# Kernel tuning notes

Measured on AMD Instinct MI355X. Metric: run time of the kernel, lower is better.

## Reference

```python
import jax, jax.numpy as jnp
import numpy as np

B, N, D, H, A = 1024, 8, 256, 512, 4  # batch, num_objects, embedding_dim, hidden_dim, action_dim


def _edge_list(batch, n):
    # Fully connected (no self-loops) over n nodes, replicated per sample with offset b*n.
    pairs = np.array([(i, j) for i in range(n) for j in range(n) if i != j], dtype=np.int32)
    off = (np.arange(batch, dtype=np.int32) * n)[:, None]
    row = (pairs[:, 0][None, :] + off).reshape(-1)
    col = (pairs[:, 1][None, :] + off).reshape(-1)
    return jnp.asarray(row), jnp.asarray(col)


def _layer_norm(x, g, b):
    m = x.mean(-1, keepdims=True)
    v = x.var(-1, keepdims=True)
    return (x - m) / jnp.sqrt(v + 1e-5) * g + b


def _mlp(x, w1, b1, w2, b2, g, bn, w3, b3):
    h = jax.nn.relu(x @ w1 + b1)
    h = jax.nn.relu(_layer_norm(h @ w2 + b2, g, bn))
    return h @ w3 + b3


def setup_inputs() -> dict:
    key = jax.random.key(0)
    ks = jax.random.split(key, 12)
    def w(k, shape):
        return jax.random.normal(k, shape, jnp.float32) / np.sqrt(shape[0]).astype(np.float32)
    return {
        "states": jax.random.normal(ks[0], (B, N, D), jnp.float32),
        "action": jax.random.randint(ks[1], (B,), 0, A),
        # edge MLP: 3D -> H -> H (LN) -> H
        "e_w1": w(ks[2], (3 * D, H)), "e_b1": jnp.zeros((H,), jnp.float32),
        "e_w2": w(ks[3], (H, H)),     "e_b2": jnp.zeros((H,), jnp.float32),
        "e_g":  jnp.ones((H,), jnp.float32), "e_bn": jnp.zeros((H,), jnp.float32),
        "e_w3": w(ks[4], (H, H)),     "e_b3": jnp.zeros((H,), jnp.float32),
        # node MLP: H + D + A -> H -> H (LN) -> D
        "n_w1": w(ks[5], (H + D + A, H)), "n_b1": jnp.zeros((H,), jnp.float32),
        "n_w2": w(ks[6], (H, H)),         "n_b2": jnp.zeros((H,), jnp.float32),
        "n_g":  jnp.ones((H,), jnp.float32), "n_bn": jnp.zeros((H,), jnp.float32),
        "n_w3": w(ks[7], (H, D)),         "n_b3": jnp.zeros((D,), jnp.float32),
    }


def reference(states, action,
              e_w1, e_b1, e_w2, e_b2, e_g, e_bn, e_w3, e_b3,
              n_w1, n_b1, n_w2, n_b2, n_g, n_bn, n_w3, n_b3):
    eP = (e_w1, e_b1, e_w2, e_b2, e_g, e_bn, e_w3, e_b3)
    nP = (n_w1, n_b1, n_w2, n_b2, n_g, n_bn, n_w3, n_b3)
    flat = states.reshape(-1, D)                       # [B*N, D]
    row, col = _edge_list(B, N - 1)                    # faithful: edge list over N-1 objects
    E = row.shape[0]
    # copy_action / embodied: one-hot action repeated per object
    av = jnp.repeat(jax.nn.one_hot(action, A, dtype=flat.dtype), N, axis=0)  # [B*N, A]
    # round 0: edge_attr starts as zeros like node features
    e = _mlp(jnp.concatenate([flat[row], jnp.zeros((E, D), flat.dtype), flat[col]], 1), *eP)
    agg = jax.ops.segment_sum(e, row, num_segments=B * N)  # [B*N, H]
    node = _mlp(jnp.concatenate([flat, av, agg], 1), *nP)   # [B*N, D]
    flat = flat + node
    av0 = jnp.zeros_like(av)
    for _ in range(N - 1):
        e = _mlp(jnp.concatenate([flat[row], node[row], flat[col]], 1), *eP)
        agg = jax.ops.segment_sum(e, row, num_segments=B * N)
        node = _mlp(jnp.concatenate([flat, av0, agg], 1), *nP)
        flat = flat + node
    return flat.reshape(B, N, D)
```

## Files before the change

kernel.cpp:

```cpp
#include <hip/hip_runtime.h>
#include <cstddef>

typedef _Float16 f16x8 __attribute__((ext_vector_type(8)));
typedef _Float16 f16x4 __attribute__((ext_vector_type(4)));
typedef float f32x16 __attribute__((ext_vector_type(16)));
typedef unsigned short ushort_t;

#define NSEG 7168
#define NNODE 8192

enum { EP_NONE = 0, EP_BIAS = 1, EP_RAWP = 2, EP_NL1 = 3, EP_NL3 = 4 };

#define PHASE_BARRIER() do { asm volatile("s_waitcnt lgkmcnt(0)" ::: "memory"); \
                             __builtin_amdgcn_s_barrier(); } while (0)

#define RELU8(v) do { _Pragma("unroll") \
  for (int j_ = 0; j_ < 8; ++j_) v[j_] = v[j_] > (_Float16)0 ? v[j_] : (_Float16)0; } while (0)

__global__ __launch_bounds__(256)
void prepack(const float* __restrict__ W, ushort_t* __restrict__ P,
             int koff, int kcnt, int Nsrc, int NTpack, int noff) {
  int idx = blockIdx.x * 256 + threadIdx.x;
  if (idx >= kcnt * Nsrc) return;
  int kl = idx / Nsrc, n = idx - kl * Nsrc + noff;
  _Float16 h = (_Float16)W[idx];
  int k = koff + kl;
  size_t o = ((((size_t)(k >> 4)) * NTpack + (n >> 5)) * 64 + ((k >> 3) & 1) * 32 + (n & 31)) * 8 + (k & 7);
  P[o] = __builtin_bit_cast(ushort_t, h);
}

__global__ __launch_bounds__(256)
void v6k(const float* __restrict__ eb3, const float* __restrict__ nw1,
         float* __restrict__ v6) {
  int n = blockIdx.x * 256 + threadIdx.x;
  if (n >= 512) return;
  float a = 0.f;
  for (int k = 0; k < 512; ++k) a += eb3[k] * nw1[(size_t)(260 + k) * 512 + n];
  v6[n] = 6.f * a;
}

template <int NCOLB, int EPI, int EDGE, int LNIN, int X1F16, int OUTF16>
__global__ __launch_bounds__(256, 4)
void gemmT(const void* __restrict__ X1v, int ld1, int nph1,
           const void* __restrict__ X2v, int ld2, int nph2,
           const ushort_t* __restrict__ Sm, const ushort_t* __restrict__ Tm,
           const ushort_t* __restrict__ P,
           const float* __restrict__ bias, const float* __restrict__ bias2,
           const int* __restrict__ action, const float* __restrict__ wact,
           const float* __restrict__ lnpart,
           const float* __restrict__ lng, const float* __restrict__ lnbn,
           void* __restrict__ Yv, float* __restrict__ Yres,
           float* __restrict__ Part, int m0base) {
  constexpr int N = NCOLB * 128;
  constexpr int NT = N / 32;
  const int u = threadIdx.x;
  const int nwg = gridDim.x;
  const int qq = nwg >> 3, r8 = nwg & 7;
  const int xcd = blockIdx.x & 7, inx = blockIdx.x >> 3;
  const int logical = (xcd < r8 ? xcd * (qq + 1) : r8 * (qq + 1) + (xcd - r8) * qq) + inx;
  const int mY = (logical / NCOLB) * 64;
  const int cb = logical - (logical / NCOLB) * NCOLB;
  const int nB = cb * 128;
  const int lane = u & 63, w = u >> 6;
  const int wr = w >> 1, wc = w & 1;
  const int r31 = lane & 31, rt2 = lane >> 5;

  __shared__ ushort_t lA[16384];
  __shared__ int eR[64], eC[64];

  if (EDGE) {
    if (u < 64) {
      int e = m0base + mY + u;
      int b = e / 42, p = e - b * 42;
      int i = p / 6, tt = p - i * 6;
      int j = tt + (tt >= i ? 1 : 0);
      eR[u] = b * 7 + i;
      eC[u] = b * 7 + j;
    }
    __syncthreads();
  }

  const int kcA = w * 2, kcB = w * 2 + 1;
  const int widx0 = (((rt2 * 8 + kcA) * 2 + 0) * 32 + (r31 ^ ((kcA & 3) << 3))) * 8;
  const int widx1 = (((rt2 * 8 + kcA) * 2 + 1) * 32 + (r31 ^ ((kcA & 3) << 3))) * 8;
  const int widx2 = (((rt2 * 8 + kcB) * 2 + 0) * 32 + (r31 ^ ((kcB & 3) << 3))) * 8;
  const int widx3 = (((rt2 * 8 + kcB) * 2 + 1) * 32 + (r31 ^ ((kcB & 3) << 3))) * 8;

  const ushort_t* sB = nullptr;
  const ushort_t* tB = nullptr;
  const float* x1f = nullptr;
  const ushort_t* x1h = nullptr;
  const ushort_t* x2h = nullptr;
  if (EDGE) {
    sB = Sm + (size_t)eR[lane] * 1024 + w * 32;
    tB = Tm + (size_t)eC[lane] * 1024 + w * 32;
  } else {
    if (X1F16) x1h = (const ushort_t*)X1v + (size_t)(mY + lane) * ld1 + w * 32;
    else       x1f = (const float*)X1v + (size_t)(mY + lane) * ld1 + w * 32;
    if (nph2 > 0) x2h = (const ushort_t*)X2v + (size_t)(mY + lane) * ld2 + w * 32;
  }
  float mym = 0.f, myr = 0.f;
  if (LNIN) {
    const float* pp = lnpart + (size_t)(mY + lane) * 16;
    float S_ = 0.f, Q_ = 0.f;
    #pragma unroll
    for (int i = 0; i < 8; ++i) { S_ += pp[i]; Q_ += pp[8 + i]; }
    mym = S_ * (1.f / 512.f);
    myr = rsqrtf(Q_ * (1.f / 512.f) - mym * mym + 1e-5f);
  }

  f16x8 xc0, xc1, xc2, xc3;
  auto loadx = [&](int ph) {
    if (EDGE) {
      const ushort_t* sp = sB + ph * 128;
      const ushort_t* tp = tB + ph * 128;
      f16x8 s0 = *(const f16x8*)sp,        t0 = *(const f16x8*)tp;
      f16x8 s1 = *(const f16x8*)(sp + 8),  t1 = *(const f16x8*)(tp + 8);
      f16x8 s2 = *(const f16x8*)(sp + 16), t2 = *(const f16x8*)(tp + 16);
      f16x8 s3 = *(const f16x8*)(sp + 24), t3 = *(const f16x8*)(tp + 24);
      xc0 = s0 + t0; xc1 = s1 + t1; xc2 = s2 + t2; xc3 = s3 + t3;
      RELU8(xc0); RELU8(xc1); RELU8(xc2); RELU8(xc3);
    } else if (!X1F16 && ph < nph1) {
      const float* src = x1f + ph * 128;
      float4 l0 = *(const float4*)(src +  0), h0 = *(const float4*)(src +  4);
      float4 l1 = *(const float4*)(src +  8), h1 = *(const float4*)(src + 12);
      float4 l2 = *(const float4*)(src + 16), h2 = *(const float4*)(src + 20);
      float4 l3 = *(const float4*)(src + 24), h3 = *(const float4*)(src + 28);
#define CVT8(X, lo, hi) do { X[0]=(_Float16)lo.x; X[1]=(_Float16)lo.y; \
      X[2]=(_Float16)lo.z; X[3]=(_Float16)lo.w; X[4]=(_Float16)hi.x; \
      X[5]=(_Float16)hi.y; X[6]=(_Float16)hi.z; X[7]=(_Float16)hi.w; } while (0)
      CVT8(xc0, l0, h0); CVT8(xc1, l1, h1); CVT8(xc2, l2, h2); CVT8(xc3, l3, h3);
#undef CVT8
    } else {
      const ushort_t* src = (ph < nph1) ? x1h + ph * 128 : x2h + (ph - nph1) * 128;
      xc0 = *(const f16x8*)src;
      xc1 = *(const f16x8*)(src + 8);
      xc2 = *(const f16x8*)(src + 16);
      xc3 = *(const f16x8*)(src + 24);
      if (LNIN) {
        const int kb = ph * 128 + w * 32;
#define LN8(X, OFS) do { _Pragma("unroll") for (int j_ = 0; j_ < 8; ++j_) { \
        float xx = (float)X[j_]; \
        xx = fmaxf((xx - mym) * myr * lng[kb + (OFS) + j_] + lnbn[kb + (OFS) + j_], 0.f); \
        X[j_] = (_Float16)xx; } } while (0)
        LN8(xc0, 0); LN8(xc1, 8); LN8(xc2, 16); LN8(xc3, 24);
#undef LN8
      }
    }
  };
  auto cvtwrite = [&](int b) {
    const int base = b * 8192;
    *(f16x8*)&lA[base + widx0] = xc0;
    *(f16x8*)&lA[base + widx1] = xc1;
    *(f16x8*)&lA[base + widx2] = xc2;
    *(f16x8*)&lA[base + widx3] = xc3;
  };

  f32x16 acc0, acc1;
  #pragma unroll
  for (int q = 0; q < 16; ++q) { acc0[q] = 0.f; acc1[q] = 0.f; }

  const int nph = nph1 + nph2;
  const int ntb = (nB >> 5) + wc * 2;
  const int TOT = nph * 8;

#define LOADA(S, A_) do { \
    const int aofs_ = lbase + (((wr * 8 + (S)) * 2 + rt2) * 32 + (r31 ^ (((S) & 3) << 3))) * 8; \
    A_ = *(const f16x8*)&lA[aofs_]; } while (0)

#define LOADB(G_, H0, H1) do { \
    const ushort_t* bp_ = P + (((size_t)(G_) * NT + ntb) * 64 + lane) * 8; \
    H0 = *(const f16x8*)bp_; \
    H1 = *(const f16x8*)(bp_ + 512); } while (0)

#define MFMA2(AH, H0, H1) do { \
    acc0 = __builtin_amdgcn_mfma_f32_32x32x16_f16(AH, H0, acc0, 0, 0, 0); \
    acc1 = __builtin_amdgcn_mfma_f32_32x32x16_f16(AH, H1, acc1, 0, 0, 0); } while (0)

  loadx(0);
  cvtwrite(0);
  if (nph > 1) loadx(1);
  PHASE_BARRIER();
  f16x8 b00, b01, b10, b11, b20, b21, b30, b31;
  LOADB(0, b00, b01);
  LOADB(1, b10, b11);
  LOADB(2, b20, b21);
  LOADB(3, b30, b31);

  #pragma unroll 1
  for (int ph = 0; ph < nph; ++ph) {
    if (ph + 1 < nph) {
      cvtwrite((ph + 1) & 1);
      if (ph + 2 < nph) loadx(ph + 2);
    }
    const int lbase = (ph & 1) * 8192;
    const int g0 = ph * 8;
    f16x8 ac, an;
    LOADA(0, ac);
#define STEP(S, BH, BL) do { \
    if ((S) < 7) LOADA((S) + 1, an); \
    f16x8 h0 = BH, h1 = BL; \
    if (g0 + (S) + 4 < TOT) LOADB(g0 + (S) + 4, BH, BL); \
    MFMA2(ac, h0, h1); \
    if ((S) < 7) ac = an; } while (0)
    STEP(0, b00, b01);
    STEP(1, b10, b11);
    STEP(2, b20, b21);
    STEP(3, b30, b31);
    STEP(4, b00, b01);
    STEP(5, b10, b11);
    STEP(6, b20, b21);
    STEP(7, b30, b31);
#undef STEP
    if (ph + 1 < nph) PHASE_BARRIER();
  }

  const int col0 = nB + wc * 64 + r31;
  float v[2][16];
  {
    float bc0 = (EPI == EP_NONE) ? 0.f : bias[col0];
    float bc1 = (EPI == EP_NONE) ? 0.f : bias[col0 + 32];
    #pragma unroll
    for (int q = 0; q < 16; ++q) {
      v[0][q] = acc0[q] + bc0;
      v[1][q] = acc1[q] + bc1;
    }
  }

  if (EPI == EP_NL1) {
    #pragma unroll
    for (int q = 0; q < 16; ++q) {
      int m = mY + wr * 32 + (q & 3) + 8 * (q >> 2) + 4 * rt2;
      if (m < NSEG) {
        v[0][q] += bias2[col0];
        v[1][q] += bias2[col0 + 32];
      }
      if (action != nullptr) {
        const float* wrp = wact + (size_t)(256 + action[m >> 3]) * 512;
        v[0][q] += wrp[col0];
        v[1][q] += wrp[col0 + 32];
      }
    }
    #pragma unroll
    for (int ct = 0; ct < 2; ++ct)
      #pragma unroll
      for (int q = 0; q < 16; ++q) v[ct][q] = fmaxf(v[ct][q], 0.f);
  }

  if (EPI == EP_RAWP) {
    float sv[16], qv[16];
    #pragma unroll
    for (int q = 0; q < 16; ++q) {
      sv[q] = v[0][q] + v[1][q];
      qv[q] = v[0][q] * v[0][q] + v[1][q] * v[1][q];
    }
    #pragma unroll
    for (int mm = 1; mm <= 16; mm <<= 1) {
      #pragma unroll
      for (int q = 0; q < 16; ++q) {
        sv[q] += __shfl_xor(sv[q], mm);
        qv[q] += __shfl_xor(qv[q], mm);
      }
    }
    if (r31 == 0) {
      #pragma unroll
      for (int q = 0; q < 16; ++q) {
        int m = mY + wr * 32 + (q & 3) + 8 * (q >> 2) + 4 * rt2;
        Part[(size_t)m * 16 + cb * 2 + wc] = sv[q];
        Part[(size_t)m * 16 + 8 + cb * 2 + wc] = qv[q];
      }
    }
  }

  #pragma unroll
  for (int ct = 0; ct < 2; ++ct) {
    #pragma unroll
    for (int q = 0; q < 16; ++q) {
      int m = mY + wr * 32 + (q & 3) + 8 * (q >> 2) + 4 * rt2;
      float z = v[ct][q];
      if (OUTF16)
        ((ushort_t*)Yv)[(size_t)m * N + col0 + ct * 32] =
            __builtin_bit_cast(ushort_t, (_Float16)z);
      else
        ((float*)Yv)[(size_t)m * N + col0 + ct * 32] = z;
      if (EPI == EP_NL3) Yres[(size_t)m * N + col0 + ct * 32] += z;
    }
  }
#undef LOADA
#undef LOADB
#undef MFMA2
}

__global__ __launch_bounds__(256)
void h2_sum_ln(const ushort_t* __restrict__ H2, const float* __restrict__ Part,
               const float* __restrict__ g, const float* __restrict__ bn,
               ushort_t* __restrict__ SS) {
  __shared__ float smu[12], srs[12];
  const int u = threadIdx.x;
  const int g2 = blockIdx.x * 2;
  if (u < 12) {
    const float* pp = Part + ((size_t)g2 * 6 + u) * 16;
    float S = 0.f, Q = 0.f;
    #pragma unroll
    for (int i = 0; i < 8; ++i) { S += pp[i]; Q += pp[8 + i]; }
    float m = S * (1.f / 512.f);
    smu[u] = m;
    srs[u] = rsqrtf(Q * (1.f / 512.f) - m * m + 1e-5f);
  }
  __syncthreads();
  const int ln = g2 + (u >> 7);
  const int lloc = (u >> 7) * 6;
  const int c4 = (u & 127) * 4;
  float4 gv = *(const float4*)(g + c4);
  float4 bv = *(const float4*)(bn + c4);
  float a0 = 0.f, a1 = 0.f, a2 = 0.f, a3 = 0.f;
  #pragma unroll
  for (int r = 0; r < 6; ++r) {
    int row = ln * 6 + r;
    f16x4 y = *(const f16x4*)(H2 + (size_t)row * 512 + c4);
    float m = smu[lloc + r], rs = srs[lloc + r];
    a0 += fmaxf(((float)y[0] - m) * rs * gv.x + bv.x, 0.f);
    a1 += fmaxf(((float)y[1] - m) * rs * gv.y + bv.y, 0.f);
    a2 += fmaxf(((float)y[2] - m) * rs * gv.z + bv.z, 0.f);
    a3 += fmaxf(((float)y[3] - m) * rs * gv.w + bv.w, 0.f);
  }
  f16x4 o;
  o[0] = (_Float16)a0; o[1] = (_Float16)a1; o[2] = (_Float16)a2; o[3] = (_Float16)a3;
  *(f16x4*)(SS + (size_t)ln * 512 + c4) = o;
}

extern "C" void kernel_launch(void* const* d_in, const int* in_sizes, int n_in,
                              void* d_out, int out_size, void* d_ws, size_t ws_size,
                              hipStream_t stream) {
  (void)in_sizes; (void)n_in; (void)out_size;
  const float* states = (const float*)d_in[0];
  const int* action = (const int*)d_in[1];
  const float* e_w1 = (const float*)d_in[2];
  const float* e_b1 = (const float*)d_in[3];
  const float* e_w2 = (const float*)d_in[4];
  const float* e_b2 = (const float*)d_in[5];
  const float* e_g = (const float*)d_in[6];
  const float* e_bn = (const float*)d_in[7];
  const float* e_w3 = (const float*)d_in[8];
  const float* e_b3 = (const float*)d_in[9];
  const float* n_w1 = (const float*)d_in[10];
  const float* n_b1 = (const float*)d_in[11];
  const float* n_w2 = (const float*)d_in[12];
  const float* n_b2 = (const float*)d_in[13];
  const float* n_g = (const float*)d_in[14];
  const float* n_bn = (const float*)d_in[15];
  const float* n_w3 = (const float*)d_in[16];
  const float* n_b3 = (const float*)d_in[17];

  float* flat = (float*)d_out;
  float* fp = (float*)d_ws;
  float* Mbuf = fp;  fp += 262144;
  float* v6 = fp;    fp += 512;
  float* b1ext = fp; fp += 1024;
  float* PartE = fp; fp += 688128;
  float* PartN = fp; fp += 131072;
  ushort_t* us = (ushort_t*)fp;
  ushort_t* node = us; us += 2097152;
  ushort_t* SS = us;   us += 4194304;
  ushort_t* G = us;    us += 4194304;
  ushort_t* G2 = us;   us += 4194304;
  ushort_t* STb = us;  us += 7340032;
  ushort_t* PeST = us; us += 524288;
  ushort_t* PeW2 = us; us += 262144;
  ushort_t* Ptmp = us; us += 262144;
  ushort_t* PnW1M = us; us += 393216;
  ushort_t* PnW2 = us;  us += 262144;
  ushort_t* PnW3 = us;  us += 131072;
  ushort_t* H2 = us;

  const size_t fixedB = (size_t)((char*)H2 - (char*)d_ws);
  int nc = 32;
  for (int cand = 1; cand <= 32; cand <<= 1)
    if (fixedB + (43008ull / cand) * 512ull * 2ull <= ws_size) { nc = cand; break; }
  const int spc = 1024 / nc;
  const int epc = spc * 42;

  hipMemsetAsync(PeST, 0, 524288 * 2, stream);
  prepack<<<1024, 256, 0, stream>>>(e_w1, PeST, 0, 512, 512, 32, 0);
  prepack<<<512, 256, 0, stream>>>(e_w1 + 262144, PeST, 0, 256, 512, 32, 512);
  prepack<<<1024, 256, 0, stream>>>(e_w2, PeW2, 0, 512, 512, 16, 0);
  prepack<<<1024, 256, 0, stream>>>(n_w1 + 133120, Ptmp, 0, 512, 512, 16, 0);
  prepack<<<512, 256, 0, stream>>>(n_w1, PnW1M, 0, 256, 512, 16, 0);
  prepack<<<1024, 256, 0, stream>>>(n_w2, PnW2, 0, 512, 512, 16, 0);
  prepack<<<512, 256, 0, stream>>>(n_w3, PnW3, 0, 512, 256, 8, 0);
  hipMemcpyAsync(b1ext, e_b1, 512 * 4, hipMemcpyDeviceToDevice, stream);
  hipMemsetAsync(b1ext + 512, 0, 512 * 4, stream);
  gemmT<4, EP_NONE, 0, 0, 0, 0><<<32, 256, 0, stream>>>(
      e_w3, 512, 4, nullptr, 0, 0, nullptr, nullptr, Ptmp, nullptr, nullptr,
      nullptr, nullptr, nullptr, nullptr, nullptr, Mbuf, nullptr, nullptr, 0);
  prepack<<<1024, 256, 0, stream>>>(Mbuf, PnW1M, 256, 512, 512, 16, 0);
  v6k<<<2, 256, 0, stream>>>(e_b3, n_w1, v6);
  hipMemsetAsync(SS + (size_t)NSEG * 512, 0, (size_t)(NNODE - NSEG) * 512 * 2, stream);
  hipMemcpyAsync(flat, states, (size_t)NNODE * 256 * 4, hipMemcpyDeviceToDevice, stream);

  for (int round = 0; round < 8; ++round) {
    if (round == 0)
      gemmT<8, EP_BIAS, 0, 0, 0, 1><<<896, 256, 0, stream>>>(
          flat, 256, 2, nullptr, 0, 0, nullptr, nullptr, PeST, b1ext, nullptr,
          nullptr, nullptr, nullptr, nullptr, nullptr, STb, nullptr, nullptr, 0);
    else
      gemmT<8, EP_BIAS, 0, 0, 0, 1><<<896, 256, 0, stream>>>(
          flat, 256, 2, node, 256, 2, nullptr, nullptr, PeST, b1ext, nullptr,
          nullptr, nullptr, nullptr, nullptr, nullptr, STb, nullptr, nullptr, 0);
    for (int ch = 0; ch < nc; ++ch) {
      gemmT<4, EP_RAWP, 1, 0, 0, 1><<<(epc / 64) * 4, 256, 0, stream>>>(
          nullptr, 0, 4, nullptr, 0, 0, STb, STb + 512, PeW2, e_b2, nullptr,
          nullptr, nullptr, nullptr, nullptr, nullptr,
          H2, nullptr, PartE, ch * epc);
      h2_sum_ln<<<(spc * 7) / 2, 256, 0, stream>>>(
          H2, PartE, e_g, e_bn, SS + (size_t)ch * spc * 7 * 512);
    }
    gemmT<4, EP_NL1, 0, 0, 0, 1><<<512, 256, 0, stream>>>(
        flat, 256, 2, SS, 512, 4, nullptr, nullptr, PnW1M, n_b1, v6,
        (round == 0) ? action : nullptr, n_w1,
        nullptr, nullptr, nullptr, G, nullptr, nullptr, 0);
    gemmT<4, EP_RAWP, 0, 0, 1, 1><<<512, 256, 0, stream>>>(
        G, 512, 4, nullptr, 0, 0, nullptr, nullptr, PnW2, n_b2, nullptr,
        nullptr, nullptr, nullptr, nullptr, nullptr, G2, nullptr, PartN, 0);
    gemmT<2, EP_NL3, 0, 1, 1, 1><<<256, 256, 0, stream>>>(
        G2, 512, 4, nullptr, 0, 0, nullptr, nullptr, PnW3, n_b3, nullptr,
        nullptr, nullptr, PartN, n_g, n_bn, node, flat, nullptr, 0);
  }
}
```

Before: 1.283 ms.

## Load GEMM A operands directly from global into MFMA registers, drop LDS staging

The A-operand path of the templated GEMM no longer stages tiles through double-buffered shared memory with barriers. Each lane now loads its own MFMA A fragment (8 fp16 values per 16-wide K chunk) straight from global memory, with gather, ReLU, LN and fp32-to-fp16 conversion applied inline. Phase counts become chunk counts and the host launch arguments change to match. This removes LDS writes and reads and the workgroup barriers, and raises occupancy headroom, in exchange for narrower 16-byte global loads, less coalescing, and both column-wave pairs redundantly fetching the same A rows.

```diff
diff --git a/kernel.cpp b/kernel.cpp
--- a/kernel.cpp
+++ b/kernel.cpp
@@ -10,9 +10,6 @@
 #define NNODE 8192
 
 enum { EP_NONE = 0, EP_BIAS = 1, EP_RAWP = 2, EP_NL1 = 3, EP_NL3 = 4 };
-
-#define PHASE_BARRIER() do { asm volatile("s_waitcnt lgkmcnt(0)" ::: "memory"); \
-                             __builtin_amdgcn_s_barrier(); } while (0)
 
 #define RELU8(v) do { _Pragma("unroll") \
   for (int j_ = 0; j_ < 8; ++j_) v[j_] = v[j_] > (_Float16)0 ? v[j_] : (_Float16)0; } while (0)
@@ -41,8 +38,8 @@
 
 template <int NCOLB, int EPI, int EDGE, int LNIN, int X1F16, int OUTF16>
 __global__ __launch_bounds__(256, 4)
-void gemmT(const void* __restrict__ X1v, int ld1, int nph1,
-           const void* __restrict__ X2v, int ld2, int nph2,
+void gemmT(const void* __restrict__ X1v, int ld1, int nch1,
+           const void* __restrict__ X2v, int ld2, int nch2,
            const ushort_t* __restrict__ Sm, const ushort_t* __restrict__ Tm,
            const ushort_t* __restrict__ P,
            const float* __restrict__ bias, const float* __restrict__ bias2,
@@ -64,44 +61,29 @@
   const int lane = u & 63, w = u >> 6;
   const int wr = w >> 1, wc = w & 1;
   const int r31 = lane & 31, rt2 = lane >> 5;
-
-  __shared__ ushort_t lA[16384];
-  __shared__ int eR[64], eC[64];
-
-  if (EDGE) {
-    if (u < 64) {
-      int e = m0base + mY + u;
-      int b = e / 42, p = e - b * 42;
-      int i = p / 6, tt = p - i * 6;
-      int j = tt + (tt >= i ? 1 : 0);
-      eR[u] = b * 7 + i;
-      eC[u] = b * 7 + j;
-    }
-    __syncthreads();
-  }
-
-  const int kcA = w * 2, kcB = w * 2 + 1;
-  const int widx0 = (((rt2 * 8 + kcA) * 2 + 0) * 32 + (r31 ^ ((kcA & 3) << 3))) * 8;
-  const int widx1 = (((rt2 * 8 + kcA) * 2 + 1) * 32 + (r31 ^ ((kcA & 3) << 3))) * 8;
-  const int widx2 = (((rt2 * 8 + kcB) * 2 + 0) * 32 + (r31 ^ ((kcB & 3) << 3))) * 8;
-  const int widx3 = (((rt2 * 8 + kcB) * 2 + 1) * 32 + (r31 ^ ((kcB & 3) << 3))) * 8;
-
-  const ushort_t* sB = nullptr;
-  const ushort_t* tB = nullptr;
+  const int myrow = mY + wr * 32 + r31;
+  const int kofs = rt2 * 8;
+
+  const ushort_t* sA = nullptr;
+  const ushort_t* tA = nullptr;
   const float* x1f = nullptr;
   const ushort_t* x1h = nullptr;
   const ushort_t* x2h = nullptr;
   if (EDGE) {
-    sB = Sm + (size_t)eR[lane] * 1024 + w * 32;
-    tB = Tm + (size_t)eC[lane] * 1024 + w * 32;
+    int e = m0base + myrow;
+    int b = e / 42, p = e - b * 42;
+    int i = p / 6, tt = p - i * 6;
+    int j = tt + (tt >= i ? 1 : 0);
+    sA = Sm + (size_t)(b * 7 + i) * 1024 + kofs;
+    tA = Tm + (size_t)(b * 7 + j) * 1024 + kofs;
   } else {
-    if (X1F16) x1h = (const ushort_t*)X1v + (size_t)(mY + lane) * ld1 + w * 32;
-    else       x1f = (const float*)X1v + (size_t)(mY + lane) * ld1 + w * 32;
-    if (nph2 > 0) x2h = (const ushort_t*)X2v + (size_t)(mY + lane) * ld2 + w * 32;
+    if (X1F16) x1h = (const ushort_t*)X1v + (size_t)myrow * ld1 + kofs;
+    else       x1f = (const float*)X1v + (size_t)myrow * ld1 + kofs;
+    if (nch2 > 0) x2h = (const ushort_t*)X2v + (size_t)myrow * ld2 + kofs;
   }
   float mym = 0.f, myr = 0.f;
   if (LNIN) {
-    const float* pp = lnpart + (size_t)(mY + lane) * 16;
+    const float* pp = lnpart + (size_t)myrow * 16;
     float S_ = 0.f, Q_ = 0.f;
     #pragma unroll
     for (int i = 0; i < 8; ++i) { S_ += pp[i]; Q_ += pp[8 + i]; }
@@ -109,64 +91,42 @@
     myr = rsqrtf(Q_ * (1.f / 512.f) - mym * mym + 1e-5f);
   }
 
-  f16x8 xc0, xc1, xc2, xc3;
-  auto loadx = [&](int ph) {
+  auto loadA = [&](int c) -> f16x8 {
+    f16x8 r;
     if (EDGE) {
-      const ushort_t* sp = sB + ph * 128;
-      const ushort_t* tp = tB + ph * 128;
-      f16x8 s0 = *(const f16x8*)sp,        t0 = *(const f16x8*)tp;
-      f16x8 s1 = *(const f16x8*)(sp + 8),  t1 = *(const f16x8*)(tp + 8);
-      f16x8 s2 = *(const f16x8*)(sp + 16), t2 = *(const f16x8*)(tp + 16);
-      f16x8 s3 = *(const f16x8*)(sp + 24), t3 = *(const f16x8*)(tp + 24);
-      xc0 = s0 + t0; xc1 = s1 + t1; xc2 = s2 + t2; xc3 = s3 + t3;
-      RELU8(xc0); RELU8(xc1); RELU8(xc2); RELU8(xc3);
-    } else if (!X1F16 && ph < nph1) {
-      const float* src = x1f + ph * 128;
-      float4 l0 = *(const float4*)(src +  0), h0 = *(const float4*)(src +  4);
-      float4 l1 = *(const float4*)(src +  8), h1 = *(const float4*)(src + 12);
-      float4 l2 = *(const float4*)(src + 16), h2 = *(const float4*)(src + 20);
-      float4 l3 = *(const float4*)(src + 24), h3 = *(const float4*)(src + 28);
-#define CVT8(X, lo, hi) do { X[0]=(_Float16)lo.x; X[1]=(_Float16)lo.y; \
-      X[2]=(_Float16)lo.z; X[3]=(_Float16)lo.w; X[4]=(_Float16)hi.x; \
-      X[5]=(_Float16)hi.y; X[6]=(_Float16)hi.z; X[7]=(_Float16)hi.w; } while (0)
-      CVT8(xc0, l0, h0); CVT8(xc1, l1, h1); CVT8(xc2, l2, h2); CVT8(xc3, l3, h3);
-#undef CVT8
+      f16x8 s = *(const f16x8*)(sA + c * 16);
+      f16x8 t = *(const f16x8*)(tA + c * 16);
+      r = s + t;
+      RELU8(r);
+    } else if (!X1F16 && c < nch1) {
+      const float* src = x1f + c * 16;
+      float4 lo = *(const float4*)src, hi = *(const float4*)(src + 4);
+      r[0] = (_Float16)lo.x; r[1] = (_Float16)lo.y;
+      r[2] = (_Float16)lo.z; r[3] = (_Float16)lo.w;
+      r[4] = (_Float16)hi.x; r[5] = (_Float16)hi.y;
+      r[6] = (_Float16)hi.z; r[7] = (_Float16)hi.w;
     } else {
-      const ushort_t* src = (ph < nph1) ? x1h + ph * 128 : x2h + (ph - nph1) * 128;
-      xc0 = *(const f16x8*)src;
-      xc1 = *(const f16x8*)(src + 8);
-      xc2 = *(const f16x8*)(src + 16);
-      xc3 = *(const f16x8*)(src + 24);
+      const ushort_t* src = (c < nch1) ? x1h + c * 16 : x2h + (c - nch1) * 16;
+      r = *(const f16x8*)src;
       if (LNIN) {
-        const int kb = ph * 128 + w * 32;
-#define LN8(X, OFS) do { _Pragma("unroll") for (int j_ = 0; j_ < 8; ++j_) { \
-        float xx = (float)X[j_]; \
-        xx = fmaxf((xx - mym) * myr * lng[kb + (OFS) + j_] + lnbn[kb + (OFS) + j_], 0.f); \
-        X[j_] = (_Float16)xx; } } while (0)
-        LN8(xc0, 0); LN8(xc1, 8); LN8(xc2, 16); LN8(xc3, 24);
-#undef LN8
-      }
-    }
-  };
-  auto cvtwrite = [&](int b) {
-    const int base = b * 8192;
-    *(f16x8*)&lA[base + widx0] = xc0;
-    *(f16x8*)&lA[base + widx1] = xc1;
-    *(f16x8*)&lA[base + widx2] = xc2;
-    *(f16x8*)&lA[base + widx3] = xc3;
+        const int kb = c * 16 + kofs;
+        #pragma unroll
+        for (int j_ = 0; j_ < 8; ++j_) {
+          float xx = (float)r[j_];
+          xx = fmaxf((xx - mym) * myr * lng[kb + j_] + lnbn[kb + j_], 0.f);
+          r[j_] = (_Float16)xx;
+        }
+      }
+    }
+    return r;
   };
 
   f32x16 acc0, acc1;
   #pragma unroll
   for (int q = 0; q < 16; ++q) { acc0[q] = 0.f; acc1[q] = 0.f; }
 
-  const int nph = nph1 + nph2;
+  const int TOT = nch1 + nch2;
   const int ntb = (nB >> 5) + wc * 2;
-  const int TOT = nph * 8;
-
-#define LOADA(S, A_) do { \
-    const int aofs_ = lbase + (((wr * 8 + (S)) * 2 + rt2) * 32 + (r31 ^ (((S) & 3) << 3))) * 8; \
-    A_ = *(const f16x8*)&lA[aofs_]; } while (0)
 
 #define LOADB(G_, H0, H1) do { \
     const ushort_t* bp_ = P + (((size_t)(G_) * NT + ntb) * 64 + lane) * 8; \
@@ -177,42 +137,39 @@
     acc0 = __builtin_amdgcn_mfma_f32_32x32x16_f16(AH, H0, acc0, 0, 0, 0); \
     acc1 = __builtin_amdgcn_mfma_f32_32x32x16_f16(AH, H1, acc1, 0, 0, 0); } while (0)
 
-  loadx(0);
-  cvtwrite(0);
-  if (nph > 1) loadx(1);
-  PHASE_BARRIER();
   f16x8 b00, b01, b10, b11, b20, b21, b30, b31;
   LOADB(0, b00, b01);
   LOADB(1, b10, b11);
   LOADB(2, b20, b21);
   LOADB(3, b30, b31);
+  f16x8 a0 = loadA(0), a1;
 
   #pragma unroll 1
-  for (int ph = 0; ph < nph; ++ph) {
-    if (ph + 1 < nph) {
-      cvtwrite((ph + 1) & 1);
-      if (ph + 2 < nph) loadx(ph + 2);
-    }
-    const int lbase = (ph & 1) * 8192;
-    const int g0 = ph * 8;
-    f16x8 ac, an;
-    LOADA(0, ac);
-#define STEP(S, BH, BL) do { \
-    if ((S) < 7) LOADA((S) + 1, an); \
-    f16x8 h0 = BH, h1 = BL; \
-    if (g0 + (S) + 4 < TOT) LOADB(g0 + (S) + 4, BH, BL); \
-    MFMA2(ac, h0, h1); \
-    if ((S) < 7) ac = an; } while (0)
-    STEP(0, b00, b01);
-    STEP(1, b10, b11);
-    STEP(2, b20, b21);
-    STEP(3, b30, b31);
-    STEP(4, b00, b01);
-    STEP(5, b10, b11);
-    STEP(6, b20, b21);
-    STEP(7, b30, b31);
-#undef STEP
-    if (ph + 1 < nph) PHASE_BARRIER();
+  for (int c = 0; c < TOT; c += 4) {
+    a1 = loadA(c + 1);
+    {
+      f16x8 h0 = b00, h1 = b01;
+      if (c + 4 < TOT) LOADB(c + 4, b00, b01);
+      MFMA2(a0, h0, h1);
+    }
+    a0 = loadA(c + 2);
+    {
+      f16x8 h0 = b10, h1 = b11;
+      if (c + 5 < TOT) LOADB(c + 5, b10, b11);
+      MFMA2(a1, h0, h1);
+    }
+    a1 = loadA(c + 3);
+    {
+      f16x8 h0 = b20, h1 = b21;
+      if (c + 6 < TOT) LOADB(c + 6, b20, b21);
+      MFMA2(a0, h0, h1);
+    }
+    if (c + 4 < TOT) a0 = loadA(c + 4);
+    {
+      f16x8 h0 = b30, h1 = b31;
+      if (c + 7 < TOT) LOADB(c + 7, b30, b31);
+      MFMA2(a1, h0, h1);
+    }
   }
 
   const int col0 = nB + wc * 64 + r31;
@@ -286,7 +243,6 @@
       if (EPI == EP_NL3) Yres[(size_t)m * N + col0 + ct * 32] += z;
     }
   }
-#undef LOADA
 #undef LOADB
 #undef MFMA2
 }
@@ -391,7 +347,7 @@
   hipMemcpyAsync(b1ext, e_b1, 512 * 4, hipMemcpyDeviceToDevice, stream);
   hipMemsetAsync(b1ext + 512, 0, 512 * 4, stream);
   gemmT<4, EP_NONE, 0, 0, 0, 0><<<32, 256, 0, stream>>>(
-      e_w3, 512, 4, nullptr, 0, 0, nullptr, nullptr, Ptmp, nullptr, nullptr,
+      e_w3, 512, 32, nullptr, 0, 0, nullptr, nullptr, Ptmp, nullptr, nullptr,
       nullptr, nullptr, nullptr, nullptr, nullptr, Mbuf, nullptr, nullptr, 0);
   prepack<<<1024, 256, 0, stream>>>(Mbuf, PnW1M, 256, 512, 512, 16, 0);
   v6k<<<2, 256, 0, stream>>>(e_b3, n_w1, v6);
@@ -401,29 +357,29 @@
   for (int round = 0; round < 8; ++round) {
     if (round == 0)
       gemmT<8, EP_BIAS, 0, 0, 0, 1><<<896, 256, 0, stream>>>(
-          flat, 256, 2, nullptr, 0, 0, nullptr, nullptr, PeST, b1ext, nullptr,
+          flat, 256, 16, nullptr, 0, 0, nullptr, nullptr, PeST, b1ext, nullptr,
           nullptr, nullptr, nullptr, nullptr, nullptr, STb, nullptr, nullptr, 0);
     else
       gemmT<8, EP_BIAS, 0, 0, 0, 1><<<896, 256, 0, stream>>>(
-          flat, 256, 2, node, 256, 2, nullptr, nullptr, PeST, b1ext, nullptr,
+          flat, 256, 16, node, 256, 16, nullptr, nullptr, PeST, b1ext, nullptr,
           nullptr, nullptr, nullptr, nullptr, nullptr, STb, nullptr, nullptr, 0);
     for (int ch = 0; ch < nc; ++ch) {
       gemmT<4, EP_RAWP, 1, 0, 0, 1><<<(epc / 64) * 4, 256, 0, stream>>>(
-          nullptr, 0, 4, nullptr, 0, 0, STb, STb + 512, PeW2, e_b2, nullptr,
+          nullptr, 0, 32, nullptr, 0, 0, STb, STb + 512, PeW2, e_b2, nullptr,
           nullptr, nullptr, nullptr, nullptr, nullptr,
           H2, nullptr, PartE, ch * epc);
       h2_sum_ln<<<(spc * 7) / 2, 256, 0, stream>>>(
           H2, PartE, e_g, e_bn, SS + (size_t)ch * spc * 7 * 512);
     }
     gemmT<4, EP_NL1, 0, 0, 0, 1><<<512, 256, 0, stream>>>(
-        flat, 256, 2, SS, 512, 4, nullptr, nullptr, PnW1M, n_b1, v6,
+        flat, 256, 16, SS, 512, 32, nullptr, nullptr, PnW1M, n_b1, v6,
         (round == 0) ? action : nullptr, n_w1,
         nullptr, nullptr, nullptr, G, nullptr, nullptr, 0);
     gemmT<4, EP_RAWP, 0, 0, 1, 1><<<512, 256, 0, stream>>>(
-        G, 512, 4, nullptr, 0, 0, nullptr, nullptr, PnW2, n_b2, nullptr,
+        G, 512, 32, nullptr, 0, 0, nullptr, nullptr, PnW2, n_b2, nullptr,
         nullptr, nullptr, nullptr, nullptr, nullptr, G2, nullptr, PartN, 0);
     gemmT<2, EP_NL3, 0, 1, 1, 1><<<256, 256, 0, stream>>>(
-        G2, 512, 4, nullptr, 0, 0, nullptr, nullptr, PnW3, n_b3, nullptr,
+        G2, 512, 32, nullptr, 0, 0, nullptr, nullptr, PnW3, n_b3, nullptr,
         nullptr, nullptr, PartN, n_g, n_bn, node, flat, nullptr, 0);
   }
 }
```

Measured after the change: 1.672 ms. 1.3x slower.
